# Performance work log

Hardware: AMD Instinct MI355X
Metric: run time of the kernel (lower is better)

## Reference

```python
import jax, jax.numpy as jnp
import numpy as np


def setup_inputs() -> dict:
    key = jax.random.key(0)
    kx, kw = jax.random.split(key)
    x = jax.random.normal(kx, (16, 256, 128, 128), dtype=jnp.float32)
    weight = jax.random.normal(kw, (128, 256, 3, 3), dtype=jnp.float32)
    return {"x": x, "weight": weight}


def reference(x, weight):
    # alpha = mean(|W|) per output channel, shape [Cout] (matches E.squeeze())
    alpha = jnp.mean(jnp.abs(weight), axis=(1, 2, 3))
    binary_weight = jnp.sign(weight)
    binary_input = jnp.sign(x)
    out = jax.lax.conv_general_dilated(
        binary_input, binary_weight,
        window_strides=(1, 1),
        padding=((1, 1), (1, 1)),
        dimension_numbers=("NCHW", "OIHW", "NCHW"),
    )  # [N, Cout, H, W] with W == Cout by construction
    # Faithful to torch: `output * alpha` broadcasts alpha[Cout] along the
    # LAST (width) axis, which equals Cout for the chosen shapes.
    return out * alpha
```

## Files before the change

### kernel.cpp

```cpp
#include <hip/hip_runtime.h>
#include <stdint.h>

#define CIN   256
#define COUT  128
#define HH    128
#define WW    128
#define NIMG  16

typedef unsigned long long u64;
typedef unsigned int u32;
typedef unsigned short u16;
typedef u32 u32x4 __attribute__((ext_vector_type(4)));
typedef int i32x4 __attribute__((ext_vector_type(4)));
typedef int i32x16 __attribute__((ext_vector_type(16)));
typedef signed char i8;

__global__ __launch_bounds__(256) void pack_x_kernel(const float* __restrict__ x,
                                                     u64* __restrict__ px) {
    int t = blockIdx.x * 256 + threadIdx.x;
    int w = t & (WW - 1);
    int h = (t >> 7) & (HH - 1);
    int n = t >> 14;
    const float* xp = x + (size_t)n * CIN * HH * WW + (size_t)h * WW + w;
    u64 words[4];
#pragma unroll
    for (int wd = 0; wd < 4; ++wd) {
        u64 acc = 0;
#pragma unroll 16
        for (int cc = 0; cc < 64; ++cc) {
            float v = xp[(size_t)(wd * 64 + cc) * (HH * WW)];
            acc |= (u64)(v > 0.0f) << cc;
        }
        words[wd] = acc;
    }
    ulonglong2* o = reinterpret_cast<ulonglong2*>(px + (size_t)t * 4);
    o[0] = make_ulonglong2(words[0], words[1]);
    o[1] = make_ulonglong2(words[2], words[3]);
}

__global__ __launch_bounds__(256) void pack_w_kernel(const float* __restrict__ wt,
                                                     i8* __restrict__ wg,
                                                     short* __restrict__ wsum,
                                                     float* __restrict__ alpha) {
    int co = blockIdx.x;
    int c  = threadIdx.x;
    int lane = c & 63;
    int word = c >> 6;
    __shared__ u64 wsh[9][4];
    __shared__ int pct[9];
    __shared__ float red[4];
    const float* wp = wt + ((size_t)co * CIN + c) * 9;
    float asum = 0.0f;
#pragma unroll
    for (int k = 0; k < 9; ++k) {
        float v = wp[k];
        asum += fabsf(v);
        u64 m = __ballot(v > 0.0f);
        if (lane == 0) wsh[k][word] = m;
        int k16g = k * 16 + (c >> 4);
        wg[((size_t)k16g * COUT + co) * 16 + (c & 15)] = (v > 0.0f) ? (i8)1 : (i8)-1;
    }
    for (int off = 32; off > 0; off >>= 1) asum += __shfl_down(asum, off);
    if (lane == 0) red[word] = asum;
    __syncthreads();
    if (c < 9)
        pct[c] = __popcll(wsh[c][0]) + __popcll(wsh[c][1]) +
                 __popcll(wsh[c][2]) + __popcll(wsh[c][3]);
    if (c == 0) alpha[co] = (red[0] + red[1] + red[2] + red[3]) * (1.0f / 2304.0f);
    __syncthreads();
    if (c < 9) {
        int pat = c, ht = pat / 3, wtp = pat % 3;
        int s = 0;
#pragma unroll
        for (int k = 0; k < 9; ++k) {
            int dh = k / 3 - 1, dw = k % 3 - 1;
            bool inv = (dh == -1 && ht == 0) || (dh == 1 && ht == 2) ||
                       (dw == -1 && wtp == 0) || (dw == 1 && wtp == 2);
            if (!inv) s += 2 * pct[k] - 256;
        }
        wsum[pat * COUT + co] = (short)s;
    }
}

__device__ __forceinline__ i32x4 spread16(u32 v) {
    u32 o0 = __umul24((v      ) & 15u, 0x00204081u) & 0x01010101u;
    u32 o1 = __umul24((v >>  4) & 15u, 0x00204081u) & 0x01010101u;
    u32 o2 = __umul24((v >>  8) & 15u, 0x00204081u) & 0x01010101u;
    u32 o3 = __umul24((v >> 12) & 15u, 0x00204081u) & 0x01010101u;
    i32x4 r = {(int)o0, (int)o1, (int)o2, (int)o3};
    return r;
}

__global__ __launch_bounds__(512, 6) void conv_kernel(const u64* __restrict__ px,
                                                      const i8* __restrict__ wg,
                                                      const short* __restrict__ wsum,
                                                      const float* __restrict__ alpha,
                                                      float* __restrict__ out) {
    __shared__ u16 xlt[3][16][130];
    __shared__ short wsl[9 * COUT];
    __shared__ float alds[WW];

    int tid = threadIdx.x;
    int bid = blockIdx.x;
    int h = bid & (HH - 1);
    int n = bid >> 7;

    if (tid < WW) alds[tid] = alpha[tid];
    {
        const u32* s = reinterpret_cast<const u32*>(wsum);
        u32* d = reinterpret_cast<u32*>(wsl);
        for (int i = tid; i < 9 * COUT / 2; i += 512) d[i] = s[i];
    }

    for (int t = tid; t < 390; t += 512) {
        int r = (t >= 260) ? 2 : ((t >= 130) ? 1 : 0);
        int p = t - r * 130;
        int gh = h - 1 + r;
        u32 bw[8] = {0, 0, 0, 0, 0, 0, 0, 0};
        if ((p >= 1) && (p <= 128) && (gh >= 0) && (gh < HH)) {
            const u32x4* s = reinterpret_cast<const u32x4*>(
                px + (size_t)((n * HH + gh) * WW + (p - 1)) * 4);
            u32x4 a = s[0], b = s[1];
            bw[0] = a.x; bw[1] = a.y; bw[2] = a.z; bw[3] = a.w;
            bw[4] = b.x; bw[5] = b.y; bw[6] = b.z; bw[7] = b.w;
        }
#pragma unroll
        for (int k16 = 0; k16 < 16; ++k16)
            xlt[r][k16][p] = (u16)(bw[k16 >> 1] >> ((k16 & 1) * 16));
    }
    __syncthreads();

    int lane = tid & 63;
    int wave = tid >> 6;
    int l31 = lane & 31;
    int hi  = lane >> 5;
    int co0  = (wave & 1) * 64;
    int pos0 = (wave >> 1) * 32;

    i32x16 acc0 = {}, acc1 = {};

#pragma unroll 1
    for (int ch = 0; ch < 18; ++ch) {
        int tap = ch >> 1;
        int k16b = (ch & 1) * 8;
        int r   = tap / 3;
        int dwi = tap - r * 3;
        int col = pos0 + l31 + dwi;
#pragma unroll
        for (int ks = 0; ks < 4; ++ks) {
            int k16 = k16b + ks * 2 + hi;
            i32x4 xf = spread16((u32)xlt[r][k16][col]);
            int k16g = tap * 16 + k16;
            const i32x4* wp = reinterpret_cast<const i32x4*>(
                wg + ((size_t)k16g * COUT) * 16);
            i32x4 wf0 = wp[co0 + l31];
            i32x4 wf1 = wp[co0 + 32 + l31];
            acc0 = __builtin_amdgcn_mfma_i32_32x32x32_i8(wf0, xf, acc0, 0, 0, 0);
            acc1 = __builtin_amdgcn_mfma_i32_32x32x32_i8(wf1, xf, acc1, 0, 0, 0);
        }
    }

    int hpat = (h == 0) ? 0 : ((h == HH - 1) ? 2 : 1);
    int wcol = pos0 + l31;
    float aw = alds[wcol];
    int wpat = (wcol == 0) ? 0 : ((wcol == WW - 1) ? 2 : 1);
    const short* wsp = &wsl[(hpat * 3 + wpat) * COUT];
    float* ob = out + ((size_t)n * COUT * HH + h) * WW + wcol;
#pragma unroll
    for (int reg = 0; reg < 16; ++reg) {
        int rr = (reg & 3) + 8 * (reg >> 2) + 4 * hi;
        int coa = co0 + rr;
        int cob = co0 + 32 + rr;
        ob[(size_t)coa * (HH * WW)] = (float)(2 * acc0[reg] - (int)wsp[coa]) * aw;
        ob[(size_t)cob * (HH * WW)] = (float)(2 * acc1[reg] - (int)wsp[cob]) * aw;
    }
}

extern "C" void kernel_launch(void* const* d_in, const int* in_sizes, int n_in,
                              void* d_out, int out_size, void* d_ws, size_t ws_size,
                              hipStream_t stream) {
    const float* x  = (const float*)d_in[0];
    const float* wt = (const float*)d_in[1];
    float* out = (float*)d_out;

    char* ws = (char*)d_ws;
    const size_t PX_BYTES = (size_t)NIMG * HH * WW * 4 * sizeof(u64);
    const size_t WG_BYTES = (size_t)144 * COUT * 16;
    const size_t WS_BYTES = (size_t)9 * COUT * sizeof(short);
    const size_t AL_BYTES = 512;
    if (ws_size < PX_BYTES + WG_BYTES + WS_BYTES + AL_BYTES) return;
    u64*   px    = (u64*)ws;
    i8*    wg    = (i8*)(ws + PX_BYTES);
    short* wsum  = (short*)(ws + PX_BYTES + WG_BYTES);
    float* alpha = (float*)(ws + PX_BYTES + WG_BYTES + WS_BYTES);

    pack_x_kernel<<<NIMG * HH * WW / 256, 256, 0, stream>>>(x, px);
    pack_w_kernel<<<COUT, 256, 0, stream>>>(wt, wg, wsum, alpha);
    conv_kernel<<<NIMG * HH, 512, 0, stream>>>(px, wg, wsum, alpha, out);
}
```

Baseline: 162.9 us.

## Compute two output rows per block with larger per-wave register tiles

Each conv block now covers two output rows instead of one, staging four input rows in LDS and running 256 threads. Each wave computes a 64-channel by 64-position tile for both rows, holding eight accumulators, so every weight fragment loaded from global memory feeds four MFMAs instead of one. This cuts weight reloads and duplicated input-row staging. In exchange it uses far more accumulator registers, halves the block count and lowers occupancy, which could expose latency.

```diff
diff --git a/kernel.cpp b/kernel.cpp
--- a/kernel.cpp
+++ b/kernel.cpp
@@ -91,31 +91,32 @@
     return r;
 }
 
-__global__ __launch_bounds__(512, 6) void conv_kernel(const u64* __restrict__ px,
+__global__ __launch_bounds__(256, 2) void conv_kernel(const u64* __restrict__ px,
                                                       const i8* __restrict__ wg,
                                                       const short* __restrict__ wsum,
                                                       const float* __restrict__ alpha,
                                                       float* __restrict__ out) {
-    __shared__ u16 xlt[3][16][130];
+    __shared__ u16 xlt[4][16][130];
     __shared__ short wsl[9 * COUT];
     __shared__ float alds[WW];
 
     int tid = threadIdx.x;
     int bid = blockIdx.x;
-    int h = bid & (HH - 1);
-    int n = bid >> 7;
+    int hpair = bid & 63;
+    int h0 = hpair << 1;
+    int n = bid >> 6;
 
     if (tid < WW) alds[tid] = alpha[tid];
     {
         const u32* s = reinterpret_cast<const u32*>(wsum);
         u32* d = reinterpret_cast<u32*>(wsl);
-        for (int i = tid; i < 9 * COUT / 2; i += 512) d[i] = s[i];
-    }
-
-    for (int t = tid; t < 390; t += 512) {
-        int r = (t >= 260) ? 2 : ((t >= 130) ? 1 : 0);
+        for (int i = tid; i < 9 * COUT / 2; i += 256) d[i] = s[i];
+    }
+
+    for (int t = tid; t < 520; t += 256) {
+        int r = t / 130;
         int p = t - r * 130;
-        int gh = h - 1 + r;
+        int gh = h0 - 1 + r;
         u32 bw[8] = {0, 0, 0, 0, 0, 0, 0, 0};
         if ((p >= 1) && (p <= 128) && (gh >= 0) && (gh < HH)) {
             const u32x4* s = reinterpret_cast<const u32x4*>(
@@ -135,9 +136,10 @@
     int l31 = lane & 31;
     int hi  = lane >> 5;
     int co0  = (wave & 1) * 64;
-    int pos0 = (wave >> 1) * 32;
-
-    i32x16 acc0 = {}, acc1 = {};
+    int pos0 = (wave >> 1) * 64;
+
+    i32x16 a0cA = {}, a0cB = {}, a0dA = {}, a0dB = {};
+    i32x16 a1cA = {}, a1cB = {}, a1dA = {}, a1dB = {};
 
 #pragma unroll 1
     for (int ch = 0; ch < 18; ++ch) {
@@ -145,35 +147,56 @@
         int k16b = (ch & 1) * 8;
         int r   = tap / 3;
         int dwi = tap - r * 3;
-        int col = pos0 + l31 + dwi;
+        int colA = pos0 + l31 + dwi;
+        int colB = colA + 32;
 #pragma unroll
         for (int ks = 0; ks < 4; ++ks) {
             int k16 = k16b + ks * 2 + hi;
-            i32x4 xf = spread16((u32)xlt[r][k16][col]);
+            i32x4 x0A = spread16((u32)xlt[r][k16][colA]);
+            i32x4 x0B = spread16((u32)xlt[r][k16][colB]);
+            i32x4 x1A = spread16((u32)xlt[r + 1][k16][colA]);
+            i32x4 x1B = spread16((u32)xlt[r + 1][k16][colB]);
             int k16g = tap * 16 + k16;
             const i32x4* wp = reinterpret_cast<const i32x4*>(
                 wg + ((size_t)k16g * COUT) * 16);
             i32x4 wf0 = wp[co0 + l31];
             i32x4 wf1 = wp[co0 + 32 + l31];
-            acc0 = __builtin_amdgcn_mfma_i32_32x32x32_i8(wf0, xf, acc0, 0, 0, 0);
-            acc1 = __builtin_amdgcn_mfma_i32_32x32x32_i8(wf1, xf, acc1, 0, 0, 0);
-        }
-    }
-
-    int hpat = (h == 0) ? 0 : ((h == HH - 1) ? 2 : 1);
-    int wcol = pos0 + l31;
-    float aw = alds[wcol];
-    int wpat = (wcol == 0) ? 0 : ((wcol == WW - 1) ? 2 : 1);
-    const short* wsp = &wsl[(hpat * 3 + wpat) * COUT];
-    float* ob = out + ((size_t)n * COUT * HH + h) * WW + wcol;
-#pragma unroll
-    for (int reg = 0; reg < 16; ++reg) {
-        int rr = (reg & 3) + 8 * (reg >> 2) + 4 * hi;
-        int coa = co0 + rr;
-        int cob = co0 + 32 + rr;
-        ob[(size_t)coa * (HH * WW)] = (float)(2 * acc0[reg] - (int)wsp[coa]) * aw;
-        ob[(size_t)cob * (HH * WW)] = (float)(2 * acc1[reg] - (int)wsp[cob]) * aw;
-    }
+            a0cA = __builtin_amdgcn_mfma_i32_32x32x32_i8(wf0, x0A, a0cA, 0, 0, 0);
+            a0cB = __builtin_amdgcn_mfma_i32_32x32x32_i8(wf0, x0B, a0cB, 0, 0, 0);
+            a0dA = __builtin_amdgcn_mfma_i32_32x32x32_i8(wf1, x0A, a0dA, 0, 0, 0);
+            a0dB = __builtin_amdgcn_mfma_i32_32x32x32_i8(wf1, x0B, a0dB, 0, 0, 0);
+            a1cA = __builtin_amdgcn_mfma_i32_32x32x32_i8(wf0, x1A, a1cA, 0, 0, 0);
+            a1cB = __builtin_amdgcn_mfma_i32_32x32x32_i8(wf0, x1B, a1cB, 0, 0, 0);
+            a1dA = __builtin_amdgcn_mfma_i32_32x32x32_i8(wf1, x1A, a1dA, 0, 0, 0);
+            a1dB = __builtin_amdgcn_mfma_i32_32x32x32_i8(wf1, x1B, a1dB, 0, 0, 0);
+        }
+    }
+
+#define STORE_TILE(ACC_C, ACC_D, ROW, WCOL)                                    \
+    {                                                                          \
+        int hh2 = h0 + (ROW);                                                  \
+        int hpat = (hh2 == 0) ? 0 : ((hh2 == HH - 1) ? 2 : 1);                 \
+        float aw = alds[(WCOL)];                                               \
+        int wpat = ((WCOL) == 0) ? 0 : (((WCOL) == WW - 1) ? 2 : 1);           \
+        const short* wsp = &wsl[(hpat * 3 + wpat) * COUT];                     \
+        float* ob = out + ((size_t)(n * COUT) * HH + hh2) * WW + (WCOL);       \
+        _Pragma("unroll")                                                      \
+        for (int reg = 0; reg < 16; ++reg) {                                   \
+            int rr = (reg & 3) + 8 * (reg >> 2) + 4 * hi;                      \
+            int coa = co0 + rr;                                                \
+            int cob = co0 + 32 + rr;                                           \
+            ob[(size_t)coa * (HH * WW)] =                                      \
+                (float)(2 * (ACC_C)[reg] - (int)wsp[coa]) * aw;                \
+            ob[(size_t)cob * (HH * WW)] =                                      \
+                (float)(2 * (ACC_D)[reg] - (int)wsp[cob]) * aw;                \
+        }                                                                      \
+    }
+
+    STORE_TILE(a0cA, a0dA, 0, pos0 + l31)
+    STORE_TILE(a0cB, a0dB, 0, pos0 + 32 + l31)
+    STORE_TILE(a1cA, a1dA, 1, pos0 + l31)
+    STORE_TILE(a1cB, a1dB, 1, pos0 + 32 + l31)
+#undef STORE_TILE
 }
 
 extern "C" void kernel_launch(void* const* d_in, const int* in_sizes, int n_in,
@@ -196,5 +219,5 @@
 
     pack_x_kernel<<<NIMG * HH * WW / 256, 256, 0, stream>>>(x, px);
     pack_w_kernel<<<COUT, 256, 0, stream>>>(wt, wg, wsum, alpha);
-    conv_kernel<<<NIMG * HH, 512, 0, stream>>>(px, wg, wsum, alpha, out);
-}
+    conv_kernel<<<NIMG * (HH / 2), 256, 0, stream>>>(px, wg, wsum, alpha, out);
+}
```

After: 158.7 us. 1.03x faster.
